# Optimization experiments

Hardware: AMD Instinct MI355X
Metric: run time of the kernel (lower is better)

The kernel has to match this reference:

```python
import jax, jax.numpy as jnp
import numpy as np

N_RAYS = 65536
N_SAMPLES = 128
N = N_RAYS * N_SAMPLES
LAMBDA_OPACITY = 1e-3
LAMBDA_DISTORTION = 1e-3


def setup_inputs() -> dict:
    key = jax.random.key(0)
    k1, k2, k3, k4, k5, k6 = jax.random.split(key, 6)
    rgb = jax.random.uniform(k1, (N_RAYS, 3), dtype=jnp.float32)
    target_rgb = jax.random.uniform(k2, (N_RAYS, 3), dtype=jnp.float32)
    opacity = jax.random.uniform(k3, (N_RAYS,), dtype=jnp.float32)
    # sample weights (small positive), interval lengths, and midpoints
    ws = jax.random.uniform(k4, (N,), dtype=jnp.float32) / N_SAMPLES
    deltas = jax.random.uniform(k5, (N,), dtype=jnp.float32) * 0.01 + 1e-4
    # ts: increasing midpoints within each ray (cumsum of positive steps per ray)
    steps = jax.random.uniform(k6, (N_RAYS, N_SAMPLES), dtype=jnp.float32) * 0.02 + 1e-3
    ts = jnp.cumsum(steps, axis=1).reshape(-1)
    ray_idx = jnp.arange(N_RAYS, dtype=jnp.int64 if jax.config.jax_enable_x64 else jnp.int32)
    rays_a = jnp.stack([ray_idx, ray_idx * N_SAMPLES,
                        jnp.full((N_RAYS,), N_SAMPLES, dtype=ray_idx.dtype)], axis=1)
    return {"rgb": rgb, "target_rgb": target_rgb, "opacity": opacity,
            "ws": ws, "deltas": deltas, "ts": ts, "rays_a": rays_a}


def _distortion_loss(ws, deltas, ts, rays_a):
    n_rays = rays_a.shape[0]
    n = ws.shape[0]
    counts = rays_a[:, 2]
    starts = rays_a[:, 1]
    # per-sample segment row ids (ragged layout), fixed total length for jit
    row_ids = jnp.repeat(jnp.arange(n_rays), counts, total_repeat_length=n)
    # segmented inclusive scans of w and w*t via global cumsum minus segment base
    prefix_w = jnp.cumsum(ws)
    prefix_wt = jnp.cumsum(ws * ts)
    base_w = jnp.where(starts > 0, prefix_w[starts - 1], 0.0)
    base_wt = jnp.where(starts > 0, prefix_wt[starts - 1], 0.0)
    W_incl = prefix_w - base_w[row_ids]    # inclusive scan of w within ray
    WT_incl = prefix_wt - base_wt[row_ids]  # inclusive scan of w*t within ray
    # loss_i = 2 w_i (t_i * sum_{j<i} w_j - sum_{j<i} w_j t_j) + (1/3) w_i^2 d_i
    per_sample = (2.0 * ws * (ts * (W_incl - ws) - (WT_incl - ws * ts))
                  + (ws * ws * deltas) / 3.0)
    per_segment = jax.ops.segment_sum(per_sample, row_ids, num_segments=n_rays)
    # scatter segment sums to their ray indices
    loss = jnp.zeros((n_rays,), dtype=ws.dtype).at[rays_a[:, 0]].add(per_segment)
    return loss


def reference(rgb, target_rgb, opacity, ws, deltas, ts, rays_a):
    d_rgb = (rgb - target_rgb) ** 2                      # (N_rays, 3)
    o = opacity + 1e-10
    d_opacity = LAMBDA_OPACITY * (-o * jnp.log(o))       # (N_rays,)
    d_distortion = LAMBDA_DISTORTION * _distortion_loss(ws, deltas, ts, rays_a)
    return d_rgb, d_opacity, d_distortion
```

## Files before the change

### kernel.cpp

```cpp
#include <hip/hip_runtime.h>
#include <math.h>

#define LAMBDA_OPACITY 0.001f
#define LAMBDA_DISTORTION 0.001f

__global__ void __launch_bounds__(256) fused_nerf_loss(
        const float* __restrict__ rgb,
        const float* __restrict__ target_rgb,
        const float* __restrict__ opacity,
        const float* __restrict__ ws,
        const float* __restrict__ deltas,
        const float* __restrict__ ts,
        const int* __restrict__ rays_a,
        float* __restrict__ out_rgb,
        float* __restrict__ out_op,
        float* __restrict__ out_dist,
        int n_rgb, int n_rays) {
    const int tid = threadIdx.x;

    if (tid < 16) {
        const int e = (blockIdx.x * 16 + tid) * 4;
        if (e < n_rgb) {
            float4 a = *reinterpret_cast<const float4*>(rgb + e);
            float4 b = *reinterpret_cast<const float4*>(target_rgb + e);
            float4 r;
            r.x = (a.x - b.x) * (a.x - b.x);
            r.y = (a.y - b.y) * (a.y - b.y);
            r.z = (a.z - b.z) * (a.z - b.z);
            r.w = (a.w - b.w) * (a.w - b.w);
            *reinterpret_cast<float4*>(out_rgb + e) = r;
        } else if (e < n_rgb + n_rays) {
            const int oi = e - n_rgb;
            float4 o = *reinterpret_cast<const float4*>(opacity + oi);
            float4 r;
            float ox = o.x + 1e-10f, oy = o.y + 1e-10f;
            float oz = o.z + 1e-10f, ow = o.w + 1e-10f;
            r.x = LAMBDA_OPACITY * (-ox * logf(ox));
            r.y = LAMBDA_OPACITY * (-oy * logf(oy));
            r.z = LAMBDA_OPACITY * (-oz * logf(oz));
            r.w = LAMBDA_OPACITY * (-ow * logf(ow));
            *reinterpret_cast<float4*>(out_op + oi) = r;
        }
    }

    const int wave = tid >> 6;
    const int lane = tid & 63;
    const int sub  = lane & 15;
    const int grp  = lane >> 4;
    const int ray  = blockIdx.x * 16 + wave * 4 + grp;
    if (ray >= n_rays) return;

    const int out_idx = rays_a[ray * 3 + 0];
    const int start   = rays_a[ray * 3 + 1];
    const int count   = rays_a[ray * 3 + 2];

    float acc = 0.f, carry_w = 0.f, carry_wt = 0.f;

    for (int base = 0; base < count; base += 128) {
        const int i0 = base + sub * 8;
        float w[8], t[8], dl[8];
        if (i0 + 8 <= count) {
            const float4 w0 = *reinterpret_cast<const float4*>(ws     + start + i0);
            const float4 w1 = *reinterpret_cast<const float4*>(ws     + start + i0 + 4);
            const float4 t0 = *reinterpret_cast<const float4*>(ts     + start + i0);
            const float4 t1 = *reinterpret_cast<const float4*>(ts     + start + i0 + 4);
            const float4 d0 = *reinterpret_cast<const float4*>(deltas + start + i0);
            const float4 d1 = *reinterpret_cast<const float4*>(deltas + start + i0 + 4);
            w[0]=w0.x; w[1]=w0.y; w[2]=w0.z; w[3]=w0.w;
            w[4]=w1.x; w[5]=w1.y; w[6]=w1.z; w[7]=w1.w;
            t[0]=t0.x; t[1]=t0.y; t[2]=t0.z; t[3]=t0.w;
            t[4]=t1.x; t[5]=t1.y; t[6]=t1.z; t[7]=t1.w;
            dl[0]=d0.x; dl[1]=d0.y; dl[2]=d0.z; dl[3]=d0.w;
            dl[4]=d1.x; dl[5]=d1.y; dl[6]=d1.z; dl[7]=d1.w;
        } else {
            #pragma unroll
            for (int k = 0; k < 8; ++k) {
                const int i = i0 + k;
                const bool v = (i < count);
                w[k]  = v ? ws[start + i]     : 0.f;
                t[k]  = v ? ts[start + i]     : 0.f;
                dl[k] = v ? deltas[start + i] : 0.f;
            }
        }

        float lw = 0.f, lwt = 0.f, cpair = 0.f, csq = 0.f;
        #pragma unroll
        for (int k = 0; k < 8; ++k) {
            const float wk = w[k], tk = t[k];
            cpair += wk * (tk * lw - lwt);
            csq   += wk * wk * dl[k];
            lw  += wk;
            lwt += wk * tk;
        }

        float sw = lw, swt = lwt;
        #pragma unroll
        for (int off = 1; off < 16; off <<= 1) {
            const float pw  = __shfl_up(sw,  off, 16);
            const float pwt = __shfl_up(swt, off, 16);
            if (sub >= off) { sw += pw; swt += pwt; }
        }
        const float Pw  = sw  - lw  + carry_w;
        const float Pwt = swt - lwt + carry_wt;

        acc += 2.f * (cpair + lwt * Pw - lw * Pwt) + csq * (1.f / 3.f);

        if (base + 128 < count) {
            carry_w  += __shfl(sw,  15, 16);
            carry_wt += __shfl(swt, 15, 16);
        }
    }

    #pragma unroll
    for (int off = 1; off < 16; off <<= 1)
        acc += __shfl_xor(acc, off, 16);

    if (sub == 0)
        out_dist[out_idx] = LAMBDA_DISTORTION * acc;
}

extern "C" void kernel_launch(void* const* d_in, const int* in_sizes, int n_in,
                              void* d_out, int out_size, void* d_ws, size_t ws_size,
                              hipStream_t stream) {
    const float* rgb        = (const float*)d_in[0];
    const float* target_rgb = (const float*)d_in[1];
    const float* opacity    = (const float*)d_in[2];
    const float* ws         = (const float*)d_in[3];
    const float* deltas     = (const float*)d_in[4];
    const float* ts         = (const float*)d_in[5];
    const int*   rays_a     = (const int*)d_in[6];

    const int n_rgb  = in_sizes[0];
    const int n_rays = in_sizes[2];

    float* out      = (float*)d_out;
    float* out_rgb  = out;
    float* out_op   = out + n_rgb;
    float* out_dist = out + n_rgb + n_rays;

    const int blocks = (n_rays + 15) / 16;
    fused_nerf_loss<<<blocks, 256, 0, stream>>>(
        rgb, target_rgb, opacity, ws, deltas, ts, rays_a,
        out_rgb, out_op, out_dist, n_rgb, n_rays);
}
```

Baseline: 21.12 us.

## Process two ray quads per wave with prefetched loads and redistributed elementwise work

Each wave now handles two quads of rays. It issues the vector loads for both before running the elementwise rgb/opacity work, so the memory latency overlaps the elementwise pass and the loads for the second quad. The grid shrinks to half the blocks, and the elementwise work is spread across all 256 threads instead of 16 per block. The cost is higher register pressure from the prefetched float4s and lower wave count, which could reduce latency hiding through occupancy.

```diff
diff --git a/kernel.cpp b/kernel.cpp
--- a/kernel.cpp
+++ b/kernel.cpp
@@ -3,6 +3,7 @@
 
 #define LAMBDA_OPACITY 0.001f
 #define LAMBDA_DISTORTION 0.001f
+
 
 __global__ void __launch_bounds__(256) fused_nerf_loss(
         const float* __restrict__ rgb,
@@ -15,108 +16,142 @@
         float* __restrict__ out_rgb,
         float* __restrict__ out_op,
         float* __restrict__ out_dist,
-        int n_rgb, int n_rays) {
-    const int tid = threadIdx.x;
-
-    if (tid < 16) {
-        const int e = (blockIdx.x * 16 + tid) * 4;
-        if (e < n_rgb) {
-            float4 a = *reinterpret_cast<const float4*>(rgb + e);
-            float4 b = *reinterpret_cast<const float4*>(target_rgb + e);
-            float4 r;
-            r.x = (a.x - b.x) * (a.x - b.x);
-            r.y = (a.y - b.y) * (a.y - b.y);
-            r.z = (a.z - b.z) * (a.z - b.z);
-            r.w = (a.w - b.w) * (a.w - b.w);
-            *reinterpret_cast<float4*>(out_rgb + e) = r;
-        } else if (e < n_rgb + n_rays) {
-            const int oi = e - n_rgb;
-            float4 o = *reinterpret_cast<const float4*>(opacity + oi);
-            float4 r;
-            float ox = o.x + 1e-10f, oy = o.y + 1e-10f;
-            float oz = o.z + 1e-10f, ow = o.w + 1e-10f;
-            r.x = LAMBDA_OPACITY * (-ox * logf(ox));
-            r.y = LAMBDA_OPACITY * (-oy * logf(oy));
-            r.z = LAMBDA_OPACITY * (-oz * logf(oz));
-            r.w = LAMBDA_OPACITY * (-ow * logf(ow));
-            *reinterpret_cast<float4*>(out_op + oi) = r;
-        }
-    }
-
+        int n_rgb, int n_rays, int n_quads, int total_waves, int ew_chunks) {
+    const int tid  = threadIdx.x;
     const int wave = tid >> 6;
     const int lane = tid & 63;
     const int sub  = lane & 15;
     const int grp  = lane >> 4;
-    const int ray  = blockIdx.x * 16 + wave * 4 + grp;
-    if (ray >= n_rays) return;
+    const int wgid = blockIdx.x * 4 + wave;
 
-    const int out_idx = rays_a[ray * 3 + 0];
-    const int start   = rays_a[ray * 3 + 1];
-    const int count   = rays_a[ray * 3 + 2];
+    const int q0 = wgid;
+    const int q1 = wgid + total_waves;
 
-    float acc = 0.f, carry_w = 0.f, carry_wt = 0.f;
+    int oi0 = 0, st0 = 0, ct0 = 0;
+    const int ray0 = q0 * 4 + grp;
+    const bool v0 = (q0 < n_quads) && (ray0 < n_rays);
+    if (v0) { oi0 = rays_a[ray0*3]; st0 = rays_a[ray0*3+1]; ct0 = rays_a[ray0*3+2]; }
 
-    for (int base = 0; base < count; base += 128) {
-        const int i0 = base + sub * 8;
-        float w[8], t[8], dl[8];
-        if (i0 + 8 <= count) {
-            const float4 w0 = *reinterpret_cast<const float4*>(ws     + start + i0);
-            const float4 w1 = *reinterpret_cast<const float4*>(ws     + start + i0 + 4);
-            const float4 t0 = *reinterpret_cast<const float4*>(ts     + start + i0);
-            const float4 t1 = *reinterpret_cast<const float4*>(ts     + start + i0 + 4);
-            const float4 d0 = *reinterpret_cast<const float4*>(deltas + start + i0);
-            const float4 d1 = *reinterpret_cast<const float4*>(deltas + start + i0 + 4);
-            w[0]=w0.x; w[1]=w0.y; w[2]=w0.z; w[3]=w0.w;
-            w[4]=w1.x; w[5]=w1.y; w[6]=w1.z; w[7]=w1.w;
-            t[0]=t0.x; t[1]=t0.y; t[2]=t0.z; t[3]=t0.w;
-            t[4]=t1.x; t[5]=t1.y; t[6]=t1.z; t[7]=t1.w;
-            dl[0]=d0.x; dl[1]=d0.y; dl[2]=d0.z; dl[3]=d0.w;
-            dl[4]=d1.x; dl[5]=d1.y; dl[6]=d1.z; dl[7]=d1.w;
-        } else {
-            #pragma unroll
-            for (int k = 0; k < 8; ++k) {
-                const int i = i0 + k;
-                const bool v = (i < count);
-                w[k]  = v ? ws[start + i]     : 0.f;
-                t[k]  = v ? ts[start + i]     : 0.f;
-                dl[k] = v ? deltas[start + i] : 0.f;
+    int oi1 = 0, st1 = 0, ct1 = 0;
+    const int ray1 = q1 * 4 + grp;
+    const bool v1 = (q1 < n_quads) && (ray1 < n_rays);
+    if (v1) { oi1 = rays_a[ray1*3]; st1 = rays_a[ray1*3+1]; ct1 = rays_a[ray1*3+2]; }
+
+    const int i0a = sub * 8;
+    const bool pf0 = v0 && (i0a + 8 <= ct0);
+    const bool pf1 = v1 && (i0a + 8 <= ct1);
+
+    float4 Aw0, Aw1, At0, At1, Ad0, Ad1;
+    float4 Bw0, Bw1, Bt0, Bt1, Bd0, Bd1;
+    if (pf0) {
+        Aw0 = *reinterpret_cast<const float4*>(ws     + st0 + i0a);
+        Aw1 = *reinterpret_cast<const float4*>(ws     + st0 + i0a + 4);
+        At0 = *reinterpret_cast<const float4*>(ts     + st0 + i0a);
+        At1 = *reinterpret_cast<const float4*>(ts     + st0 + i0a + 4);
+        Ad0 = *reinterpret_cast<const float4*>(deltas + st0 + i0a);
+        Ad1 = *reinterpret_cast<const float4*>(deltas + st0 + i0a + 4);
+    }
+    if (pf1) {
+        Bw0 = *reinterpret_cast<const float4*>(ws     + st1 + i0a);
+        Bw1 = *reinterpret_cast<const float4*>(ws     + st1 + i0a + 4);
+        Bt0 = *reinterpret_cast<const float4*>(ts     + st1 + i0a);
+        Bt1 = *reinterpret_cast<const float4*>(ts     + st1 + i0a + 4);
+        Bd0 = *reinterpret_cast<const float4*>(deltas + st1 + i0a);
+        Bd1 = *reinterpret_cast<const float4*>(deltas + st1 + i0a + 4);
+    }
+
+    {
+        const int chunk = blockIdx.x * 256 + tid;
+        if (chunk < ew_chunks) {
+            const int e = chunk * 4;
+            if (e < n_rgb) {
+                float4 a = *reinterpret_cast<const float4*>(rgb + e);
+                float4 b = *reinterpret_cast<const float4*>(target_rgb + e);
+                float4 r;
+                r.x = (a.x-b.x)*(a.x-b.x); r.y = (a.y-b.y)*(a.y-b.y);
+                r.z = (a.z-b.z)*(a.z-b.z); r.w = (a.w-b.w)*(a.w-b.w);
+                *reinterpret_cast<float4*>(out_rgb + e) = r;
+            } else if (e < n_rgb + n_rays) {
+                const int oi = e - n_rgb;
+                float4 o = *reinterpret_cast<const float4*>(opacity + oi);
+                float ox = o.x+1e-10f, oy = o.y+1e-10f, oz = o.z+1e-10f, ow = o.w+1e-10f;
+                float4 r;
+                r.x = LAMBDA_OPACITY * (-ox * logf(ox));
+                r.y = LAMBDA_OPACITY * (-oy * logf(oy));
+                r.z = LAMBDA_OPACITY * (-oz * logf(oz));
+                r.w = LAMBDA_OPACITY * (-ow * logf(ow));
+                *reinterpret_cast<float4*>(out_op + oi) = r;
             }
-        }
-
-        float lw = 0.f, lwt = 0.f, cpair = 0.f, csq = 0.f;
-        #pragma unroll
-        for (int k = 0; k < 8; ++k) {
-            const float wk = w[k], tk = t[k];
-            cpair += wk * (tk * lw - lwt);
-            csq   += wk * wk * dl[k];
-            lw  += wk;
-            lwt += wk * tk;
-        }
-
-        float sw = lw, swt = lwt;
-        #pragma unroll
-        for (int off = 1; off < 16; off <<= 1) {
-            const float pw  = __shfl_up(sw,  off, 16);
-            const float pwt = __shfl_up(swt, off, 16);
-            if (sub >= off) { sw += pw; swt += pwt; }
-        }
-        const float Pw  = sw  - lw  + carry_w;
-        const float Pwt = swt - lwt + carry_wt;
-
-        acc += 2.f * (cpair + lwt * Pw - lw * Pwt) + csq * (1.f / 3.f);
-
-        if (base + 128 < count) {
-            carry_w  += __shfl(sw,  15, 16);
-            carry_wt += __shfl(swt, 15, 16);
         }
     }
 
-    #pragma unroll
-    for (int off = 1; off < 16; off <<= 1)
-        acc += __shfl_xor(acc, off, 16);
+    #define COMPUTE_QUAD(VAL, OI, ST, CT, PF, W0, W1, T0, T1, D0, D1)          \
+    {                                                                          \
+        float acc = 0.f, carry_w = 0.f, carry_wt = 0.f;                        \
+        for (int base = 0; base < CT; base += 128) {                           \
+            const int i0 = base + sub * 8;                                     \
+            float w[8], t[8], dl[8];                                           \
+            if (base == 0 && PF) {                                             \
+                w[0]=W0.x; w[1]=W0.y; w[2]=W0.z; w[3]=W0.w;                    \
+                w[4]=W1.x; w[5]=W1.y; w[6]=W1.z; w[7]=W1.w;                    \
+                t[0]=T0.x; t[1]=T0.y; t[2]=T0.z; t[3]=T0.w;                    \
+                t[4]=T1.x; t[5]=T1.y; t[6]=T1.z; t[7]=T1.w;                    \
+                dl[0]=D0.x; dl[1]=D0.y; dl[2]=D0.z; dl[3]=D0.w;                \
+                dl[4]=D1.x; dl[5]=D1.y; dl[6]=D1.z; dl[7]=D1.w;                \
+            } else {                                                           \
+                _Pragma("unroll")                                              \
+                for (int k = 0; k < 8; ++k) {                                  \
+                    const int i = i0 + k;                                      \
+                    const bool vv = (i < CT);                                  \
+                    w[k]  = vv ? ws[ST + i]     : 0.f;                         \
+                    t[k]  = vv ? ts[ST + i]     : 0.f;                         \
+                    dl[k] = vv ? deltas[ST + i] : 0.f;                         \
+                }                                                              \
+            }                                                                  \
+            float lw = 0.f, lwt = 0.f, cpair = 0.f, csq = 0.f;                 \
+            _Pragma("unroll")                                                  \
+            for (int k = 0; k < 8; ++k) {                                      \
+                const float wk = w[k], tk = t[k];                              \
+                cpair += wk * (tk * lw - lwt);                                 \
+                csq   += wk * wk * dl[k];                                      \
+                lw  += wk;                                                     \
+                lwt += wk * tk;                                                \
+            }                                                                  \
+            float sw = lw, swt = lwt;                                          \
+            _Pragma("unroll")                                                  \
+            for (int off = 1; off < 16; off <<= 1) {                           \
+                const float pw  = __shfl_up(sw,  off, 16);                     \
+                const float pwt = __shfl_up(swt, off, 16);                     \
+                if (sub >= off) { sw += pw; swt += pwt; }                      \
+            }                                                                  \
+            const float Pw  = sw  - lw  + carry_w;                             \
+            const float Pwt = swt - lwt + carry_wt;                            \
+            acc += 2.f * (cpair + lwt * Pw - lw * Pwt) + csq * (1.f / 3.f);    \
+            if (base + 128 < CT) {                                             \
+                carry_w  += __shfl(sw,  15, 16);                               \
+                carry_wt += __shfl(swt, 15, 16);                               \
+            }                                                                  \
+        }                                                                      \
+        _Pragma("unroll")                                                      \
+        for (int off = 1; off < 16; off <<= 1)                                 \
+            acc += __shfl_xor(acc, off, 16);                                   \
+        if (VAL && sub == 0)                                                   \
+            out_dist[OI] = LAMBDA_DISTORTION * acc;                            \
+    }
 
-    if (sub == 0)
-        out_dist[out_idx] = LAMBDA_DISTORTION * acc;
+    COMPUTE_QUAD(v0, oi0, st0, ct0, pf0, Aw0, Aw1, At0, At1, Ad0, Ad1)
+    COMPUTE_QUAD(v1, oi1, st1, ct1, pf1, Bw0, Bw1, Bt0, Bt1, Bd0, Bd1)
+
+    for (int q = wgid + 2 * total_waves; q < n_quads; q += total_waves) {
+        const int ray = q * 4 + grp;
+        const bool v = (ray < n_rays);
+        int oi = 0, st = 0, ct = 0;
+        if (v) { oi = rays_a[ray*3]; st = rays_a[ray*3+1]; ct = rays_a[ray*3+2]; }
+        const bool pf = false;
+        float4 Z0, Z1;
+        COMPUTE_QUAD(v, oi, st, ct, pf, Z0, Z1, Z0, Z1, Z0, Z1)
+    }
+    #undef COMPUTE_QUAD
 }
 
 extern "C" void kernel_launch(void* const* d_in, const int* in_sizes, int n_in,
@@ -138,8 +173,15 @@
     float* out_op   = out + n_rgb;
     float* out_dist = out + n_rgb + n_rays;
 
-    const int blocks = (n_rays + 15) / 16;
+    const int n_quads   = (n_rays + 3) / 4;
+    const int ray_blocks = (n_quads + 7) / 8;
+    const int ew_chunks = (n_rgb + n_rays + 3) / 4;
+    const int ew_blocks = (ew_chunks + 255) / 256;
+    const int blocks = ray_blocks > ew_blocks ? ray_blocks : ew_blocks;
+    const int total_waves = blocks * 4;
+
     fused_nerf_loss<<<blocks, 256, 0, stream>>>(
         rgb, target_rgb, opacity, ws, deltas, ts, rays_a,
-        out_rgb, out_op, out_dist, n_rgb, n_rays);
+        out_rgb, out_op, out_dist,
+        n_rgb, n_rays, n_quads, total_waves, ew_chunks);
 }
```

Measured after the change: 22.16 us. +4.9%, slower.
